# Optimization experiments

Hardware: AMD Instinct MI355X
Metric: run time of the kernel (lower is better)

Reference implementation:

```python
import jax, jax.numpy as jnp
import numpy as np

LN_EPS = 1e-5

def _layernorm(x, g, b):
    mu = jnp.mean(x, axis=-1, keepdims=True)
    var = jnp.var(x, axis=-1, keepdims=True)
    return (x - mu) * jax.lax.rsqrt(var + LN_EPS) * g + b

def _attention(q_in, ctx, wq, wk, wv, wo, bo, n_heads):
    b, n, _ = q_in.shape
    m = ctx.shape[1]
    d_attn = wq.shape[1]
    d_head = d_attn // n_heads
    Q = (q_in @ wq).reshape(b, n, n_heads, d_head)
    K = (ctx @ wk).reshape(b, m, n_heads, d_head)
    V = (ctx @ wv).reshape(b, m, n_heads, d_head)
    scale = 1.0 / np.sqrt(d_head).astype(np.float32)
    sim = jnp.einsum('bnhd,bmhd->bhnm', Q, K) * scale
    attn = jax.nn.softmax(sim, axis=-1)
    out = jnp.einsum('bhnm,bmhd->bnhd', attn, V).reshape(b, n, d_attn)
    return out @ wo + bo

def setup_inputs() -> dict:
    key = jax.random.key(0)
    ks = jax.random.split(key, 16)
    B, N, D = 8, 1024, 640
    M, CD = 77, 768
    H = 4 * D  # GEGLU hidden = 2560
    s = lambda d: 1.0 / np.sqrt(d)
    return {
        'x': jax.random.normal(ks[0], (B, N, D), jnp.float32),
        'context': jax.random.normal(ks[1], (B, M, CD), jnp.float32),
        'sa_wq': jax.random.normal(ks[2], (D, D), jnp.float32) * s(D),
        'sa_wk': jax.random.normal(ks[3], (D, D), jnp.float32) * s(D),
        'sa_wv': jax.random.normal(ks[4], (D, D), jnp.float32) * s(D),
        'sa_wo': jax.random.normal(ks[5], (D, D), jnp.float32) * s(D),
        'sa_bo': jnp.zeros((D,), jnp.float32),
        'ca_wq': jax.random.normal(ks[6], (D, D), jnp.float32) * s(D),
        'ca_wk': jax.random.normal(ks[7], (CD, D), jnp.float32) * s(CD),
        'ca_wv': jax.random.normal(ks[8], (CD, D), jnp.float32) * s(CD),
        'ca_wo': jax.random.normal(ks[9], (D, D), jnp.float32) * s(D),
        'ca_bo': jnp.zeros((D,), jnp.float32),
        'ff_w1': jax.random.normal(ks[10], (D, 2 * H), jnp.float32) * s(D),
        'ff_b1': jnp.zeros((2 * H,), jnp.float32),
        'ff_w2': jax.random.normal(ks[11], (H, D), jnp.float32) * s(H),
        'ff_b2': jnp.zeros((D,), jnp.float32),
        'ln1_g': jnp.ones((D,), jnp.float32), 'ln1_b': jnp.zeros((D,), jnp.float32),
        'ln2_g': jnp.ones((D,), jnp.float32), 'ln2_b': jnp.zeros((D,), jnp.float32),
        'ln3_g': jnp.ones((D,), jnp.float32), 'ln3_b': jnp.zeros((D,), jnp.float32),
    }

def reference(x, context, sa_wq, sa_wk, sa_wv, sa_wo, sa_bo,
              ca_wq, ca_wk, ca_wv, ca_wo, ca_bo,
              ff_w1, ff_b1, ff_w2, ff_b2,
              ln1_g, ln1_b, ln2_g, ln2_b, ln3_g, ln3_b):
    n_heads = 8
    # post-norm residual block, matching norm_i(x + sublayer(x))
    x = _layernorm(x + _attention(x, x, sa_wq, sa_wk, sa_wv, sa_wo, sa_bo, n_heads), ln1_g, ln1_b)
    x = _layernorm(x + _attention(x, context, ca_wq, ca_wk, ca_wv, ca_wo, ca_bo, n_heads), ln2_g, ln2_b)
    h = x @ ff_w1 + ff_b1
    a, gate = jnp.split(h, 2, axis=-1)
    ff = (a * jax.nn.gelu(gate, approximate=False)) @ ff_w2 + ff_b2
    x = _layernorm(x + ff, ln3_g, ln3_b)
    return x
```

## Files before the change

kernel.cpp:

```cpp
#include <hip/hip_runtime.h>


using u16 = unsigned short;
typedef __attribute__((ext_vector_type(8))) short bfrag;
typedef __attribute__((ext_vector_type(4))) float f4;
typedef __attribute__((ext_vector_type(4))) unsigned short us4;

#define MFMA(a, b, c) __builtin_amdgcn_mfma_f32_16x16x32_bf16((a), (b), (c), 0, 0, 0)

__device__ __forceinline__ void gload16(const void* g, void* l) {
    __builtin_amdgcn_global_load_lds(
        (const __attribute__((address_space(1))) void*)g,
        (__attribute__((address_space(3))) void*)l, 16, 0, 0);
}

__device__ __forceinline__ u16 f2b(float f) {
    unsigned u = __float_as_uint(f);
    unsigned r = u + 0x7FFFu + ((u >> 16) & 1u);
    return (u16)(r >> 16);
}
__device__ __forceinline__ float b2f(u16 u) {
    return __uint_as_float(((unsigned)u) << 16);
}
__device__ __forceinline__ unsigned pack2(float a, float b) {
    return (unsigned)f2b(a) | ((unsigned)f2b(b) << 16);
}
__device__ __forceinline__ bfrag bzero() {
    bfrag z = {0,0,0,0,0,0,0,0};
    return z;
}
__device__ __forceinline__ float gelu_f(float x) {
    float y = 0.7978845608028654f * (x + 0.044715f * x * x * x);
    float e = exp2f(y * 2.8853900817779268f);
    float t = 1.0f - 2.0f * __builtin_amdgcn_rcpf(e + 1.0f);
    return 0.5f * x * (1.0f + t);
}

__device__ __forceinline__ void transp_tile(const float* __restrict__ in,
                                            u16* __restrict__ out,
                                            int K, int N, int ldo,
                                            int tile, bool perm,
                                            float (*t)[33])
{
    int nw = N >> 5;
    int n0 = (tile % nw) * 32, k0 = (tile / nw) * 32;
    int tx = threadIdx.x & 31, ty = threadIdx.x >> 5;
    #pragma unroll
    for (int i = 0; i < 32; i += 8)
        t[ty + i][tx] = in[(size_t)(k0 + ty + i) * N + n0 + tx];
    __syncthreads();
    #pragma unroll
    for (int i = 0; i < 32; i += 8) {
        int n = n0 + ty + i;
        int dst;
        if (perm) {
            dst = (n < 2560) ? ((n >> 5) * 64 + (n & 31))
                             : (((n - 2560) >> 5) * 64 + 32 + ((n - 2560) & 31));
        } else {
            dst = n;
        }
        out[(size_t)dst * ldo + k0 + tx] = f2b(t[tx][ty + i]);
    }
}

__global__ __launch_bounds__(256) void prep_k(
    const float* __restrict__ x, const float* __restrict__ ctx,
    const float* __restrict__ sa_wq, const float* __restrict__ sa_wk,
    const float* __restrict__ sa_wv, const float* __restrict__ sa_wo,
    const float* __restrict__ ca_wq, const float* __restrict__ ca_wk,
    const float* __restrict__ ca_wv, const float* __restrict__ ca_wo,
    const float* __restrict__ ff_w1, const float* __restrict__ ff_w2,
    u16* saqkvt, u16* sawot, u16* cawqt, u16* cawot, u16* cakvt,
    u16* ffw1t, u16* ffw2t, u16* xb, u16* ctxb)
{
    __shared__ float t[32][33];
    int b = blockIdx.x;
    if (b < 2400) {
        int task = b / 400, tile = b - task * 400;
        const float* src;
        u16* dst;
        if      (task == 0) { src = sa_wq; dst = saqkvt; }
        else if (task == 1) { src = sa_wk; dst = saqkvt + 409600; }
        else if (task == 2) { src = sa_wv; dst = saqkvt + 819200; }
        else if (task == 3) { src = sa_wo; dst = sawot; }
        else if (task == 4) { src = ca_wq; dst = cawqt; }
        else                { src = ca_wo; dst = cawot; }
        transp_tile(src, dst, 640, 640, 640, tile, false, t);
    } else if (b < 3360) {
        int tt = b - 2400;
        int task = tt / 480, tile = tt - task * 480;
        transp_tile(task ? ca_wv : ca_wk, cakvt + task * 491520, 768, 640, 768,
                    tile, false, t);
    } else if (b < 6560) {
        transp_tile(ff_w1, ffw1t, 640, 5120, 640, b - 3360, true, t);
    } else if (b < 8160) {
        transp_tile(ff_w2, ffw2t, 2560, 640, 2560, b - 6560, false, t);
    } else if (b < 10720) {
        int i = (b - 8160) * 256 + threadIdx.x;
        const float4* p = (const float4*)x + (size_t)i * 2;
        float4 a = p[0], bb = p[1];
        uint4 w = { pack2(a.x, a.y), pack2(a.z, a.w),
                    pack2(bb.x, bb.y), pack2(bb.z, bb.w) };
        ((uint4*)xb)[i] = w;
    } else {
        int i = (b - 10720) * 256 + threadIdx.x;
        int rowOut = i / 96, c8 = (i - rowOut * 96) * 8;
        int bb = rowOut / 80, r = rowOut - bb * 80;
        uint4 w = {0, 0, 0, 0};
        if (r < 77) {
            const float4* p = (const float4*)(ctx + ((size_t)(bb * 77 + r)) * 768 + c8);
            float4 a = p[0], b2 = p[1];
            w = (uint4){ pack2(a.x, a.y), pack2(a.z, a.w),
                         pack2(b2.x, b2.y), pack2(b2.z, b2.w) };
        }
        ((uint4*)ctxb)[i] = w;
    }
}

template<int MODE>
__device__ __forceinline__ void gemm_core(const u16* __restrict__ A,
                                          const u16* __restrict__ Bt,
                                          int N, int K, int ld,
                                          const float* __restrict__ bias,
                                          const u16* __restrict__ resb,
                                          float* __restrict__ outf,
                                          u16* __restrict__ outb,
                                          u16* __restrict__ out2,
                                          int bx, int by,
                                          u16* As, u16* Bs)
{
    const int lane = threadIdx.x & 63;
    const int wid  = threadIdx.x >> 6;
    const int q    = lane >> 4;
    const int lc   = lane & 15;
    const int wm = wid >> 1, wn = wid & 1;
    const int m0 = by * 128;
    const int n0 = bx * 128;
    const int ldb = ld * 2;

    f4 acc[4][4];
    #pragma unroll
    for (int i = 0; i < 4; ++i)
        #pragma unroll
        for (int j = 0; j < 4; ++j) acc[i][j] = (f4){0.f, 0.f, 0.f, 0.f};

    const char* Abase = (const char*)A + (size_t)m0 * ldb;
    const char* Bbase = (const char*)Bt + (size_t)n0 * ldb;

    for (int kt = 0; kt < K; kt += 64) {
        #pragma unroll
        for (int c = 0; c < 4; ++c) {
            int cid = wid * 4 + c;
            int o = cid * 1024 + lane * 16;
            int row = o >> 7;
            int pc  = o & 127;
            int src = pc ^ ((row & 7) << 4);
            gload16(Abase + (size_t)row * ldb + kt * 2 + src, (char*)As + cid * 1024);
            gload16(Bbase + (size_t)row * ldb + kt * 2 + src, (char*)Bs + cid * 1024);
        }
        __syncthreads();
        #pragma unroll
        for (int ks = 0; ks < 2; ++ks) {
            bfrag a[4], b[4];
            #pragma unroll
            for (int mi = 0; mi < 4; ++mi) {
                int row = wm * 64 + mi * 16 + lc;
                int off = row * 128 + ((ks * 64 + q * 16) ^ ((row & 7) << 4));
                a[mi] = *(const bfrag*)((const char*)As + off);
            }
            #pragma unroll
            for (int ni = 0; ni < 4; ++ni) {
                int row = wn * 64 + ni * 16 + lc;
                int off = row * 128 + ((ks * 64 + q * 16) ^ ((row & 7) << 4));
                b[ni] = *(const bfrag*)((const char*)Bs + off);
            }
            #pragma unroll
            for (int mi = 0; mi < 4; ++mi)
                #pragma unroll
                for (int ni = 0; ni < 4; ++ni)
                    acc[mi][ni] = MFMA(a[mi], b[ni], acc[mi][ni]);
        }
        __syncthreads();
    }

    const int baseRow = m0 + wm * 64;
    const int baseCol = n0 + wn * 64;

    if (MODE == 4) {
        const int blk = baseCol >> 6;
        #pragma unroll
        for (int mi = 0; mi < 4; ++mi)
            #pragma unroll
            for (int ni = 0; ni < 2; ++ni) {
                int j = blk * 32 + ni * 16 + lc;
                float ba = bias[j];
                float bg = bias[2560 + j];
                #pragma unroll
                for (int r = 0; r < 4; ++r) {
                    int row = baseRow + mi * 16 + q * 4 + r;
                    float aa = acc[mi][ni][r] + ba;
                    float gg = acc[mi][ni + 2][r] + bg;
                    outb[(size_t)row * 2560 + j] = f2b(aa * gelu_f(gg));
                }
            }
        return;
    }

    #pragma unroll
    for (int mi = 0; mi < 4; ++mi)
        #pragma unroll
        for (int ni = 0; ni < 4; ++ni) {
            int col = baseCol + ni * 16 + lc;
            if (MODE == 2) {
                const float qs = (col < 640) ? 0.11180339887498949f : 1.0f;
                us4 vv = {0, 0, 0, 0};
                #pragma unroll
                for (int r = 0; r < 4; ++r) {
                    int row = baseRow + mi * 16 + q * 4 + r;
                    u16 u = f2b(acc[mi][ni][r] * qs);
                    outb[(size_t)row * 1920 + col] = u;
                    vv[r] = u;
                }
                if (col >= 1280) {
                    int cd = col - 1280;
                    int hh = cd / 80, dd = cd - hh * 80;
                    int row0 = baseRow + mi * 16 + q * 4;
                    int bb = row0 >> 10, tok = row0 & 1023;
                    *(us4*)&out2[(size_t)((bb * 8 + hh) * 80 + dd) * 1024 + tok] = vv;
                }
            } else {
                #pragma unroll
                for (int r = 0; r < 4; ++r) {
                    int row = baseRow + mi * 16 + q * 4 + r;
                    float v = acc[mi][ni][r];
                    if (MODE == 0) {
                        v += bias[col] + b2f(resb[(size_t)row * N + col]);
                        outf[(size_t)row * N + col] = v;
                    } else if (MODE == 1) {
                        outb[(size_t)row * N + col] = f2b(v);
                    } else if (MODE == 3) {
                        int bb = row / 80, rr = row - bb * 80;
                        if (rr < 77) {
                            u16 u = f2b(v);
                            if (col < 640) {
                                outb[(size_t)row * 640 + col] = u;
                            } else {
                                int cd = col - 640;
                                int hh = cd / 80, dd = cd - hh * 80;
                                out2[((bb * 8 + hh) * 80 + dd) * 80 + rr] = u;
                            }
                        }
                    }
                }
            }
        }
}

template<int MODE>
__global__ __launch_bounds__(256) void gemm_bt(const u16* __restrict__ A,
                                               const u16* __restrict__ Bt,
                                               int N, int K,
                                               const float* __restrict__ bias,
                                               const u16* __restrict__ resb,
                                               float* __restrict__ outf,
                                               u16* __restrict__ outb,
                                               u16* __restrict__ out2)
{
    __shared__ u16 As[128 * 64];
    __shared__ u16 Bs[128 * 64];
    gemm_core<MODE>(A, Bt, N, K, K, bias, resb, outf, outb, out2,
                    blockIdx.x, blockIdx.y, As, Bs);
}

__global__ __launch_bounds__(256) void gemm_qkv_cakv(
    const u16* __restrict__ xb, const u16* __restrict__ saqkvt,
    const u16* __restrict__ ctxb, const u16* __restrict__ cakvt,
    u16* qkvb, u16* vt, u16* kc, u16* vct)
{
    __shared__ u16 As[128 * 64];
    __shared__ u16 Bs[128 * 64];
    int bid = blockIdx.x;
    if (bid < 960) {
        gemm_core<2>(xb, saqkvt, 1920, 640, 640, nullptr, nullptr, nullptr,
                     qkvb, vt, bid % 15, bid / 15, As, Bs);
    } else {
        int tt = bid - 960;
        gemm_core<3>(ctxb, cakvt, 1280, 768, 768, nullptr, nullptr, nullptr,
                     kc, vct, tt % 10, tt / 10, As, Bs);
    }
}

template<int MODE>
__global__ __launch_bounds__(256) void gemm_n64(const u16* __restrict__ A,
                                                const u16* __restrict__ Bt,
                                                int N, int K,
                                                const float* __restrict__ bias,
                                                const u16* __restrict__ resb,
                                                float* __restrict__ outf,
                                                u16* __restrict__ outb)
{
    __shared__ u16 As[128 * 64];
    __shared__ u16 Bs[64 * 64];
    const int lane = threadIdx.x & 63;
    const int wid  = threadIdx.x >> 6;
    const int hi   = lane >> 4;
    const int lc   = lane & 15;
    const int wm = wid >> 1, wn = wid & 1;
    const int m0 = blockIdx.y * 128;
    const int n0 = blockIdx.x * 64;
    const int ldb = K * 2;

    f4 acc[4][2];
    #pragma unroll
    for (int i = 0; i < 4; ++i)
        #pragma unroll
        for (int j = 0; j < 2; ++j) acc[i][j] = (f4){0.f, 0.f, 0.f, 0.f};

    const char* Abase = (const char*)A + (size_t)m0 * ldb;
    const char* Bbase = (const char*)Bt + (size_t)n0 * ldb;

    for (int kt = 0; kt < K; kt += 64) {
        #pragma unroll
        for (int c = 0; c < 6; ++c) {
            int cid = wid * 6 + c;
            if (cid < 16) {
                int o = cid * 1024 + lane * 16;
                int row = o >> 7;
                int src = (o & 127) ^ ((row & 7) << 4);
                gload16(Abase + (size_t)row * ldb + kt * 2 + src, (char*)As + cid * 1024);
            } else {
                int c2 = cid - 16;
                int o = c2 * 1024 + lane * 16;
                int row = o >> 7;
                int src = (o & 127) ^ ((row & 7) << 4);
                gload16(Bbase + (size_t)row * ldb + kt * 2 + src, (char*)Bs + c2 * 1024);
            }
        }
        __syncthreads();
        #pragma unroll
        for (int ks = 0; ks < 2; ++ks) {
            bfrag a[4], b[2];
            #pragma unroll
            for (int mi = 0; mi < 4; ++mi) {
                int row = wm * 64 + mi * 16 + lc;
                int off = row * 128 + ((ks * 64 + hi * 16) ^ ((row & 7) << 4));
                a[mi] = *(const bfrag*)((const char*)As + off);
            }
            #pragma unroll
            for (int ni = 0; ni < 2; ++ni) {
                int row = wn * 32 + ni * 16 + lc;
                int off = row * 128 + ((ks * 64 + hi * 16) ^ ((row & 7) << 4));
                b[ni] = *(const bfrag*)((const char*)Bs + off);
            }
            #pragma unroll
            for (int mi = 0; mi < 4; ++mi)
                #pragma unroll
                for (int ni = 0; ni < 2; ++ni)
                    acc[mi][ni] = MFMA(a[mi], b[ni], acc[mi][ni]);
        }
        __syncthreads();
    }

    const int baseRow = m0 + wm * 64;
    const int baseCol = n0 + wn * 32;
    #pragma unroll
    for (int mi = 0; mi < 4; ++mi)
        #pragma unroll
        for (int ni = 0; ni < 2; ++ni) {
            int col = baseCol + ni * 16 + lc;
            #pragma unroll
            for (int r = 0; r < 4; ++r) {
                int row = baseRow + mi * 16 + hi * 4 + r;
                float v = acc[mi][ni][r];
                if (MODE == 0) {
                    v += bias[col] + b2f(resb[(size_t)row * N + col]);
                    outf[(size_t)row * N + col] = v;
                } else {
                    outb[(size_t)row * N + col] = f2b(v);
                }
            }
        }
}

__global__ __launch_bounds__(256) void attn_sa(const u16* __restrict__ qkv,
                                               const u16* __restrict__ vt,
                                               u16* __restrict__ out)
{
    __shared__ u16 Qs[64 * 80];
    __shared__ u16 Ks[64 * 80];
    __shared__ u16 Vs[80 * 64];
    __shared__ u16 Ps[4][16 * 64];

    const int lane = threadIdx.x & 63;
    const int wid  = threadIdx.x >> 6;
    const int hi   = lane >> 4;
    const int lc   = lane & 15;
    const int bid = blockIdx.x;
    const int qt = bid >> 6;
    const int bb = (bid >> 3) & 7;
    const int hh = bid & 7;
    const int tok0 = bb * 1024 + qt * 64;
    const char* qbase = (const char*)qkv;

    for (int c = wid; c < 10; c += 4) {
        int o = c * 1024 + lane * 16;
        int row = o / 160, col = o - row * 160;
        gload16(qbase + (size_t)(tok0 + row) * 3840 + hh * 160 + col, (char*)Qs + c * 1024);
    }
    __syncthreads();

    const int qrow = wid * 16 + lc;
    bfrag qf0 = *(const bfrag*)((const char*)Qs + qrow * 160 + hi * 16);
    bfrag qf1 = *(const bfrag*)((const char*)Qs + qrow * 160 + 64 + hi * 16);
    bfrag qf2 = bzero();
    if (hi < 2) qf2 = *(const bfrag*)((const char*)Qs + qrow * 160 + 128 + hi * 16);

    float m = -3e30f, l = 0.f;
    f4 accO[5];
    #pragma unroll
    for (int no = 0; no < 5; ++no) accO[no] = (f4){0.f, 0.f, 0.f, 0.f};

    const float L2E = 1.4426950408889634f;

    for (int t = 0; t < 16; ++t) {
        __syncthreads();
        for (int c = wid; c < 20; c += 4) {
            if (c < 10) {
                int o = c * 1024 + lane * 16;
                int row = o / 160, col = o - row * 160;
                gload16(qbase + (size_t)(bb * 1024 + t * 64 + row) * 3840 + 1280 + hh * 160 + col,
                        (char*)Ks + c * 1024);
            } else {
                int c2 = c - 10;
                int o = c2 * 1024 + lane * 16;
                int row = o >> 7;
                int pc  = o & 127;
                int src = pc ^ ((row & 7) << 4);
                gload16((const char*)vt + (size_t)((bb * 8 + hh) * 80 + row) * 2048 + t * 128 + src,
                        (char*)Vs + c2 * 1024);
            }
        }
        __syncthreads();

        f4 sT[4];
        #pragma unroll
        for (int nb = 0; nb < 4; ++nb) {
            const char* kb = (const char*)Ks + (nb * 16 + lc) * 160;
            bfrag k0 = *(const bfrag*)(kb + hi * 16);
            bfrag k1 = *(const bfrag*)(kb + 64 + hi * 16);
            bfrag k2 = bzero();
            if (hi < 2) k2 = *(const bfrag*)(kb + 128 + hi * 16);
            f4 a = {0.f, 0.f, 0.f, 0.f};
            a = MFMA(k0, qf0, a);
            a = MFMA(k1, qf1, a);
            a = MFMA(k2, qf2, a);
            sT[nb] = a;
        }

        float pm = sT[0][0];
        #pragma unroll
        for (int nb = 0; nb < 4; ++nb)
            #pragma unroll
            for (int r = 0; r < 4; ++r) pm = fmaxf(pm, sT[nb][r]);
        pm = fmaxf(pm, __shfl_xor(pm, 16));
        pm = fmaxf(pm, __shfl_xor(pm, 32));

        if (__any(pm > m + 8.0f)) {
            float mn = fmaxf(m, pm);
            float al = exp2f((m - mn) * L2E);
            m = mn;
            l *= al;
            float af[4];
            #pragma unroll
            for (int r = 0; r < 4; ++r) af[r] = __shfl(al, hi * 4 + r);
            #pragma unroll
            for (int no = 0; no < 5; ++no)
                #pragma unroll
                for (int r = 0; r < 4; ++r) accO[no][r] *= af[r];
        }

        float sum = 0.f;
        #pragma unroll
        for (int nb = 0; nb < 4; ++nb)
            #pragma unroll
            for (int r = 0; r < 4; ++r) {
                float p = exp2f((sT[nb][r] - m) * L2E);
                sT[nb][r] = p;
                sum += p;
            }
        sum += __shfl_xor(sum, 16);
        sum += __shfl_xor(sum, 32);
        l += sum;

        char* Pw = (char*)&Ps[wid][0];
        #pragma unroll
        for (int nb = 0; nb < 4; ++nb) {
            us4 pk = { f2b(sT[nb][0]), f2b(sT[nb][1]), f2b(sT[nb][2]), f2b(sT[nb][3]) };
            int cb = (nb * 16 + hi * 4) * 2;
            *(us4*)(Pw + lc * 128 + (cb ^ ((lc & 7) << 4))) = pk;
        }

        bfrag pa0 = *(const bfrag*)(Pw + lc * 128 + ((hi * 16) ^ ((lc & 7) << 4)));
        bfrag pa1 = *(const bfrag*)(Pw + lc * 128 + ((64 + hi * 16) ^ ((lc & 7) << 4)));
        #pragma unroll
        for (int no = 0; no < 5; ++no) {
            int vr = no * 16 + lc;
            const char* vb = (const char*)Vs + vr * 128;
            bfrag v0 = *(const bfrag*)(vb + ((hi * 16) ^ ((vr & 7) << 4)));
            bfrag v1 = *(const bfrag*)(vb + ((64 + hi * 16) ^ ((vr & 7) << 4)));
            accO[no] = MFMA(pa0, v0, accO[no]);
            accO[no] = MFMA(pa1, v1, accO[no]);
        }
    }

    float rf[4];
    #pragma unroll
    for (int r = 0; r < 4; ++r) {
        float lf = __shfl(l, hi * 4 + r);
        rf[r] = __builtin_amdgcn_rcpf(lf);
    }
    #pragma unroll
    for (int no = 0; no < 5; ++no)
        #pragma unroll
        for (int r = 0; r < 4; ++r) {
            int row = tok0 + wid * 16 + hi * 4 + r;
            int col = hh * 80 + no * 16 + lc;
            out[(size_t)row * 640 + col] = f2b(accO[no][r] * rf[r]);
        }
}

__global__ __launch_bounds__(256) void attn_ca(const u16* __restrict__ qc,
                                               const u16* __restrict__ kc,
                                               const u16* __restrict__ vct,
                                               u16* __restrict__ out)
{
    __shared__ u16 Qs[64 * 80];
    __shared__ u16 Ks[84 * 80];
    __shared__ u16 Vs[84 * 80];
    __shared__ u16 Ps[4][16 * 80];

    const int lane = threadIdx.x & 63;
    const int wid  = threadIdx.x >> 6;
    const int q    = lane >> 4;
    const int lc   = lane & 15;
    const int bid = blockIdx.x;
    const int qt = bid & 15;
    const int hh = (bid >> 4) & 7;
    const int bb = bid >> 7;
    const int tok0 = bb * 1024 + qt * 64;

    for (int c = wid; c < 36; c += 4) {
        if (c < 10) {
            int o = c * 1024 + lane * 16;
            int row = o / 160, col = o - row * 160;
            gload16((const char*)qc + (size_t)(tok0 + row) * 1280 + hh * 160 + col,
                    (char*)Qs + c * 1024);
        } else if (c < 23) {
            int c2 = c - 10;
            int o = c2 * 1024 + lane * 16;
            int row = o / 160, col = o - row * 160;
            gload16((const char*)kc + (size_t)(bb * 80 + row) * 1280 + hh * 160 + col,
                    (char*)Ks + c2 * 1024);
        } else {
            int c2 = c - 23;
            int o = c2 * 1024 + lane * 16;
            int row = o / 160, col = o - row * 160;
            gload16((const char*)vct + (size_t)((bb * 8 + hh) * 80 + row) * 160 + col,
                    (char*)Vs + c2 * 1024);
        }
    }
    __syncthreads();

    const int qrow = wid * 16 + lc;
    bfrag qf0 = *(const bfrag*)((const char*)Qs + qrow * 160 + q * 16);
    bfrag qf1 = *(const bfrag*)((const char*)Qs + qrow * 160 + 64 + q * 16);
    bfrag qf2 = bzero();
    if (q < 2) qf2 = *(const bfrag*)((const char*)Qs + qrow * 160 + 128 + q * 16);

    const float SC = 0.11180339887498949f;
    const float L2E = 1.4426950408889634f;

    f4 s[5];
    #pragma unroll
    for (int nb = 0; nb < 5; ++nb) {
        const char* kb = (const char*)Ks + (nb * 16 + lc) * 160;
        bfrag k0 = *(const bfrag*)(kb + q * 16);
        bfrag k1 = *(const bfrag*)(kb + 64 + q * 16);
        bfrag k2 = bzero();
        if (q < 2) k2 = *(const bfrag*)(kb + 128 + q * 16);
        f4 a = {0.f, 0.f, 0.f, 0.f};
        a = MFMA(qf0, k0, a);
        a = MFMA(qf1, k1, a);
        a = MFMA(qf2, k2, a);
        s[nb] = a;
    }
    #pragma unroll
    for (int nb = 0; nb < 5; ++nb) {
        int key = nb * 16 + lc;
        #pragma unroll
        for (int r = 0; r < 4; ++r) {
            s[nb][r] *= SC;
            if (key >= 77) s[nb][r] = -1e30f;
        }
    }
    float mrow[4], lrow[4];
    #pragma unroll
    for (int r = 0; r < 4; ++r) {
        float v = fmaxf(fmaxf(fmaxf(s[0][r], s[1][r]), fmaxf(s[2][r], s[3][r])), s[4][r]);
        v = fmaxf(v, __shfl_xor(v, 1));
        v = fmaxf(v, __shfl_xor(v, 2));
        v = fmaxf(v, __shfl_xor(v, 4));
        v = fmaxf(v, __shfl_xor(v, 8));
        mrow[r] = v;
    }
    float rsum[4] = {0.f, 0.f, 0.f, 0.f};
    #pragma unroll
    for (int nb = 0; nb < 5; ++nb)
        #pragma unroll
        for (int r = 0; r < 4; ++r) {
            float p = exp2f((s[nb][r] - mrow[r]) * L2E);
            s[nb][r] = p;
            rsum[r] += p;
        }
    #pragma unroll
    for (int r = 0; r < 4; ++r) {
        float v = rsum[r];
        v += __shfl_xor(v, 1);
        v += __shfl_xor(v, 2);
        v += __shfl_xor(v, 4);
        v += __shfl_xor(v, 8);
        lrow[r] = v;
    }

    char* Pw = (char*)&Ps[wid][0];
    #pragma unroll
    for (int nb = 0; nb < 5; ++nb)
        #pragma unroll
        for (int r = 0; r < 4; ++r) {
            int prow = q * 4 + r;
            *(u16*)(Pw + prow * 160 + (nb * 16 + lc) * 2) = f2b(s[nb][r]);
        }
    bfrag pa0 = *(const bfrag*)(Pw + lc * 160 + q * 16);
    bfrag pa1 = *(const bfrag*)(Pw + lc * 160 + 64 + q * 16);
    bfrag pa2 = bzero();
    if (q < 2) pa2 = *(const bfrag*)(Pw + lc * 160 + 128 + q * 16);

    f4 accO[5];
    #pragma unroll
    for (int no = 0; no < 5; ++no) {
        const char* vb = (const char*)Vs + (no * 16 + lc) * 160;
        bfrag v0 = *(const bfrag*)(vb + q * 16);
        bfrag v1 = *(const bfrag*)(vb + 64 + q * 16);
        bfrag v2 = bzero();
        if (q < 2) v2 = *(const bfrag*)(vb + 128 + q * 16);
        f4 a = {0.f, 0.f, 0.f, 0.f};
        a = MFMA(pa0, v0, a);
        a = MFMA(pa1, v1, a);
        a = MFMA(pa2, v2, a);
        accO[no] = a;
    }
    #pragma unroll
    for (int no = 0; no < 5; ++no)
        #pragma unroll
        for (int r = 0; r < 4; ++r) {
            int row = tok0 + wid * 16 + q * 4 + r;
            int col = hh * 80 + no * 16 + lc;
            out[(size_t)row * 640 + col] = f2b(accO[no][r] / lrow[r]);
        }
}

__global__ __launch_bounds__(256) void ln_k(const float* __restrict__ pre,
                                            const float* __restrict__ g,
                                            const float* __restrict__ b,
                                            float* __restrict__ xo,
                                            u16* __restrict__ xb)
{
    const int lane = threadIdx.x & 63;
    const int wid  = threadIdx.x >> 6;
    const int row = blockIdx.x * 4 + wid;
    const float* p = pre + (size_t)row * 640;
    float v[10];
    #pragma unroll
    for (int i = 0; i < 10; ++i) v[i] = p[lane + i * 64];
    float s = 0.f;
    #pragma unroll
    for (int i = 0; i < 10; ++i) s += v[i];
    #pragma unroll
    for (int m = 1; m < 64; m <<= 1) s += __shfl_xor(s, m);
    float mu = s * (1.0f / 640.0f);
    float d2 = 0.f;
    #pragma unroll
    for (int i = 0; i < 10; ++i) { float d = v[i] - mu; d2 += d * d; }
    #pragma unroll
    for (int m = 1; m < 64; m <<= 1) d2 += __shfl_xor(d2, m);
    float rs = rsqrtf(d2 * (1.0f / 640.0f) + 1e-5f);
    #pragma unroll
    for (int i = 0; i < 10; ++i) {
        int col = lane + i * 64;
        float y = (v[i] - mu) * rs * g[col] + b[col];
        if (xo) xo[(size_t)row * 640 + col] = y;
        if (xb) xb[(size_t)row * 640 + col] = f2b(y);
    }
}

extern "C" void kernel_launch(void* const* d_in, const int* in_sizes, int n_in,
                              void* d_out, int out_size, void* d_ws, size_t ws_size,
                              hipStream_t stream)
{
    const float* x       = (const float*)d_in[0];
    const float* context = (const float*)d_in[1];
    const float* sa_wq = (const float*)d_in[2];
    const float* sa_wk = (const float*)d_in[3];
    const float* sa_wv = (const float*)d_in[4];
    const float* sa_wo = (const float*)d_in[5];
    const float* sa_bo = (const float*)d_in[6];
    const float* ca_wq = (const float*)d_in[7];
    const float* ca_wk = (const float*)d_in[8];
    const float* ca_wv = (const float*)d_in[9];
    const float* ca_wo = (const float*)d_in[10];
    const float* ca_bo = (const float*)d_in[11];
    const float* ff_w1 = (const float*)d_in[12];
    const float* ff_b1 = (const float*)d_in[13];
    const float* ff_w2 = (const float*)d_in[14];
    const float* ff_b2 = (const float*)d_in[15];
    const float* ln1_g = (const float*)d_in[16];
    const float* ln1_b = (const float*)d_in[17];
    const float* ln2_g = (const float*)d_in[18];
    const float* ln2_b = (const float*)d_in[19];
    const float* ln3_g = (const float*)d_in[20];
    const float* ln3_b = (const float*)d_in[21];

    char* ws = (char*)d_ws;
    const size_t OFF_XB     = 0;
    const size_t OFF_QKVB   = 10485760;
    const size_t OFF_VT     = 41943040;
    const size_t OFF_AB     = 52428800;
    const size_t OFF_ATTN   = 62914560;
    const size_t OFF_QC     = 73400320;
    const size_t OFF_KC     = 83886080;
    const size_t OFF_VCT    = 84705280;
    const size_t OFF_SAQKVT = 85524480;
    const size_t OFF_SAWOT  = 87982080;
    const size_t OFF_CAWQT  = 88801280;
    const size_t OFF_CAKVT  = 89620480;
    const size_t OFF_CAWOT  = 91586560;
    const size_t OFF_FFW1T  = 92405760;
    const size_t OFF_FFW2T  = 98959360;
    const size_t OFF_CTXB   = 102236160;
    const size_t OFF_PRE    = 103219200;

    u16* xb      = (u16*)(ws + OFF_XB);
    u16* qkvb    = (u16*)(ws + OFF_QKVB);
    u16* vt      = (u16*)(ws + OFF_VT);
    u16* ab      = (u16*)(ws + OFF_AB);
    u16* attnb   = (u16*)(ws + OFF_ATTN);
    u16* qc      = (u16*)(ws + OFF_QC);
    u16* kc      = (u16*)(ws + OFF_KC);
    u16* vct     = (u16*)(ws + OFF_VCT);
    u16* saqkvt  = (u16*)(ws + OFF_SAQKVT);
    u16* sawot   = (u16*)(ws + OFF_SAWOT);
    u16* cawqt   = (u16*)(ws + OFF_CAWQT);
    u16* cakvt   = (u16*)(ws + OFF_CAKVT);
    u16* cawot   = (u16*)(ws + OFF_CAWOT);
    u16* ffw1t   = (u16*)(ws + OFF_FFW1T);
    u16* ffw2t   = (u16*)(ws + OFF_FFW2T);
    u16* ctxb    = (u16*)(ws + OFF_CTXB);
    float* pre   = (float*)(ws + OFF_PRE);
    u16* ffh     = (u16*)(ws + OFF_XB);

    hipLaunchKernelGGL(prep_k, dim3(10960), dim3(256), 0, stream,
                       x, context, sa_wq, sa_wk, sa_wv, sa_wo, ca_wq, ca_wk,
                       ca_wv, ca_wo, ff_w1, ff_w2,
                       saqkvt, sawot, cawqt, cawot, cakvt, ffw1t, ffw2t, xb, ctxb);

    hipLaunchKernelGGL(gemm_qkv_cakv, dim3(1010), dim3(256), 0, stream,
                       xb, saqkvt, ctxb, cakvt, qkvb, vt, kc, vct);
    hipLaunchKernelGGL(attn_sa, dim3(1024), dim3(256), 0, stream, qkvb, vt, attnb);
    hipLaunchKernelGGL(gemm_n64<0>, dim3(10, 64), dim3(256), 0, stream,
                       attnb, sawot, 640, 640, sa_bo, xb, pre, (u16*)nullptr);
    hipLaunchKernelGGL(ln_k, dim3(2048), dim3(256), 0, stream, pre, ln1_g, ln1_b,
                       (float*)nullptr, ab);

    hipLaunchKernelGGL(gemm_n64<1>, dim3(10, 64), dim3(256), 0, stream,
                       ab, cawqt, 640, 640, (const float*)nullptr, (const u16*)nullptr,
                       (float*)nullptr, qc);
    hipLaunchKernelGGL(attn_ca, dim3(1024), dim3(256), 0, stream, qc, kc, vct, attnb);
    hipLaunchKernelGGL(gemm_n64<0>, dim3(10, 64), dim3(256), 0, stream,
                       attnb, cawot, 640, 640, ca_bo, ab, pre, (u16*)nullptr);
    hipLaunchKernelGGL(ln_k, dim3(2048), dim3(256), 0, stream, pre, ln2_g, ln2_b,
                       (float*)nullptr, ab);

    hipLaunchKernelGGL(gemm_bt<4>, dim3(40, 64), dim3(256), 0, stream,
                       ab, ffw1t, 5120, 640, ff_b1, (const u16*)nullptr,
                       (float*)nullptr, ffh, (u16*)nullptr);
    hipLaunchKernelGGL(gemm_bt<0>, dim3(5, 64), dim3(256), 0, stream,
                       ffh, ffw2t, 640, 2560, ff_b2, ab, pre,
                       (u16*)nullptr, (u16*)nullptr);
    hipLaunchKernelGGL(ln_k, dim3(2048), dim3(256), 0, stream, pre, ln3_g, ln3_b,
                       (float*)d_out, (u16*)nullptr);
}
```

Before: 350.3 us.

## Prefetch next K/V tile into registers in self-attention; use n64 GEMM for FF2

The self-attention kernel used to load K and V tiles straight into LDS, bracketed by two barriers on every iteration. It now loads the next tile into registers while the current tile is being computed, then writes them to LDS after a barrier. This is meant to hide global-load latency behind the MFMA and softmax work, at the cost of extra VGPRs (five uint4 per thread) and a register-to-LDS store step. The FF2 GEMM launch also switches from gemm_bt with a 5-column grid to gemm_n64 with a 10-column grid, giving smaller tiles and more blocks for the 640-wide output.

After: 411.0 us. 1.17x slower.

```diff
diff --git a/kernel.cpp b/kernel.cpp
--- a/kernel.cpp
+++ b/kernel.cpp
@@ -407,6 +407,39 @@
         int row = o / 160, col = o - row * 160;
         gload16(qbase + (size_t)(tok0 + row) * 3840 + hh * 160 + col, (char*)Qs + c * 1024);
     }
+
+    uint4 pf[5];
+    auto ldchunks = [&](int t) {
+        #pragma unroll
+        for (int i = 0; i < 5; ++i) {
+            int c = wid + i * 4;
+            if (c < 10) {
+                int o = c * 1024 + lane * 16;
+                int row = o / 160, col = o - row * 160;
+                pf[i] = *(const uint4*)(qbase
+                    + (size_t)(bb * 1024 + t * 64 + row) * 3840 + 1280 + hh * 160 + col);
+            } else {
+                int c2 = c - 10;
+                int o = c2 * 1024 + lane * 16;
+                int row = o >> 7;
+                int src = (o & 127) ^ ((row & 7) << 4);
+                pf[i] = *(const uint4*)((const char*)vt
+                    + (size_t)((bb * 8 + hh) * 80 + row) * 2048 + t * 128 + src);
+            }
+        }
+    };
+    auto stchunks = [&]() {
+        #pragma unroll
+        for (int i = 0; i < 5; ++i) {
+            int c = wid + i * 4;
+            char* d = (c < 10) ? ((char*)Ks + c * 1024)
+                               : ((char*)Vs + (c - 10) * 1024);
+            *(uint4*)(d + lane * 16) = pf[i];
+        }
+    };
+
+    ldchunks(0);
+    stchunks();
     __syncthreads();
 
     const int qrow = wid * 16 + lc;
@@ -423,24 +456,7 @@
     const float L2E = 1.4426950408889634f;
 
     for (int t = 0; t < 16; ++t) {
-        __syncthreads();
-        for (int c = wid; c < 20; c += 4) {
-            if (c < 10) {
-                int o = c * 1024 + lane * 16;
-                int row = o / 160, col = o - row * 160;
-                gload16(qbase + (size_t)(bb * 1024 + t * 64 + row) * 3840 + 1280 + hh * 160 + col,
-                        (char*)Ks + c * 1024);
-            } else {
-                int c2 = c - 10;
-                int o = c2 * 1024 + lane * 16;
-                int row = o >> 7;
-                int pc  = o & 127;
-                int src = pc ^ ((row & 7) << 4);
-                gload16((const char*)vt + (size_t)((bb * 8 + hh) * 80 + row) * 2048 + t * 128 + src,
-                        (char*)Vs + c2 * 1024);
-            }
-        }
-        __syncthreads();
+        if (t < 15) ldchunks(t + 1);
 
         f4 sT[4];
         #pragma unroll
@@ -510,6 +526,12 @@
             bfrag v1 = *(const bfrag*)(vb + ((64 + hi * 16) ^ ((vr & 7) << 4)));
             accO[no] = MFMA(pa0, v0, accO[no]);
             accO[no] = MFMA(pa1, v1, accO[no]);
+        }
+
+        __syncthreads();
+        if (t < 15) {
+            stchunks();
+            __syncthreads();
         }
     }
 
@@ -793,9 +815,8 @@
     hipLaunchKernelGGL(gemm_bt<4>, dim3(40, 64), dim3(256), 0, stream,
                        ab, ffw1t, 5120, 640, ff_b1, (const u16*)nullptr,
                        (float*)nullptr, ffh, (u16*)nullptr);
-    hipLaunchKernelGGL(gemm_bt<0>, dim3(5, 64), dim3(256), 0, stream,
-                       ffh, ffw2t, 640, 2560, ff_b2, ab, pre,
-                       (u16*)nullptr, (u16*)nullptr);
+    hipLaunchKernelGGL(gemm_n64<0>, dim3(10, 64), dim3(256), 0, stream,
+                       ffh, ffw2t, 640, 2560, ff_b2, ab, pre, (u16*)nullptr);
     hipLaunchKernelGGL(ln_k, dim3(2048), dim3(256), 0, stream, pre, ln3_g, ln3_b,
                        (float*)d_out, (u16*)nullptr);
 }
```
